# Performance work log

Measured on AMD Instinct MI355X. Metric: run time of the kernel, lower is better.

Reference implementation:

```python
import jax, jax.numpy as jnp
import numpy as np

# Detect.__init__ defaults from the source
TOP_K = 5000
CONF_THRESH = 0.01
NMS_THRESH = 0.3
VAR0, VAR1 = 0.1, 0.2   # variance = [0.1, 0.2]
NUM_CLASSES = 2

B = 16
IMAGE = 1280
FMAPS = [320, 160, 80, 40, 20, 10]          # image / steps [4,8,16,32,64,128]
MIN_SIZES = [16, 32, 64, 128, 256, 512]
AR = 1.5                                     # aspect_ratios = [[1.5]] * 6


def make_priors():
    """Vectorized PriorBox.forward: 1 prior per location (max_sizes=[], single AR)."""
    chunks = []
    for f, ms in zip(FMAPS, MIN_SIZES):
        c = (np.arange(f, dtype=np.float32) + 0.5) / f
        cy, cx = np.meshgrid(c, c, indexing='ij')
        s = ms / float(IMAGE)
        w = np.full_like(cx, s / np.sqrt(AR))   # s_k / sqrt(ar)
        h = np.full_like(cx, s * np.sqrt(AR))   # s_k * sqrt(ar)
        chunks.append(np.stack([cx, cy, w, h], -1).reshape(-1, 4))
    pr = np.concatenate(chunks, 0).clip(0.0, 1.0)   # clip=True
    return jnp.asarray(pr, jnp.float32)             # [136500, 4]


def setup_inputs() -> dict:
    key = jax.random.key(0)
    k1, k2 = jax.random.split(key)
    P = sum(f * f for f in FMAPS)   # 136500
    loc_data = 0.5 * jax.random.normal(k1, (B, P, 4), jnp.float32)
    conf_data = jax.random.uniform(k2, (B * P, NUM_CLASSES), jnp.float32)  # post-softmax probs
    prior_data = make_priors()
    return {"loc_data": loc_data, "conf_data": conf_data, "prior_data": prior_data}


def _decode(loc, priors):
    # SSD box decode with variances [0.1, 0.2]; loc, priors: [P,4]
    cxcy = priors[:, :2] + loc[:, :2] * VAR0 * priors[:, 2:]
    wh = priors[:, 2:] * jnp.exp(loc[:, 2:] * VAR1)
    xy1 = cxcy - wh * 0.5
    xy2 = xy1 + wh
    return jnp.concatenate([xy1, xy2], axis=-1)   # [P,4] x1y1x2y2


def _greedy_keep(boxes, valid):
    # Greedy NMS over score-sorted candidates. boxes [K,4], valid [K] bool.
    # Indices/keep decisions are discrete -> computed on stop_gradient'd boxes.
    b = jax.lax.stop_gradient(boxes)
    x1, y1, x2, y2 = b[:, 0], b[:, 1], b[:, 2], b[:, 3]
    area = (x2 - x1) * (y2 - y1)
    idxs = jnp.arange(b.shape[0])

    def body(keep, i):
        iw = jnp.maximum(jnp.minimum(x2, x2[i]) - jnp.maximum(x1, x1[i]), 0.0)
        ih = jnp.maximum(jnp.minimum(y2, y2[i]) - jnp.maximum(y1, y1[i]), 0.0)
        inter = iw * ih
        iou = inter / (area + area[i] - inter)
        suppress = keep[i] & (iou > NMS_THRESH) & (idxs > i)
        return keep & ~suppress, None

    keep, _ = jax.lax.scan(body, valid, idxs)
    return keep


def _detect_one(loc_i, conf_cl, priors):
    # loc_i [P,4]; conf_cl [P] = class-1 scores; returns [TOP_K, 5] (score, x1,y1,x2,y2)
    boxes = _decode(loc_i, priors)
    masked = jnp.where(conf_cl > CONF_THRESH, conf_cl, -1.0)   # c_mask gating
    order = jnp.argsort(-jax.lax.stop_gradient(masked))[:TOP_K]  # scores.sort, top_k cap
    s = masked[order]
    b = boxes[order]
    valid = s > CONF_THRESH
    keep = _greedy_keep(b, valid)
    # scatter kept (score, box) rows, in descending-score order, into dense output
    rank = jnp.cumsum(keep) - 1
    row = jnp.where(keep, rank, TOP_K)            # dropped rows -> scratch slot
    vals = jnp.concatenate([s[:, None], b], axis=1)
    vals = jnp.where(keep[:, None], vals, 0.0)
    out = jnp.zeros((TOP_K + 1, 5), jnp.float32).at[row].set(vals)
    return out[:TOP_K]


def reference(loc_data, conf_data, prior_data):
    num = loc_data.shape[0]
    P = prior_data.shape[0]
    conf_preds = conf_data.reshape(num, P, NUM_CLASSES).transpose(0, 2, 1)  # [B,2,P]
    cls1 = jax.vmap(_detect_one, in_axes=(0, 0, None))(loc_data, conf_preds[:, 1, :], prior_data)
    bg = jnp.zeros_like(cls1)                     # background class row stays zero
    output = jnp.stack([bg, cls1], axis=1)        # [B, 2, TOP_K, 5]
    # NOTE: the original's final `flt[(rank < top_k)...].fill_(0)` fills a boolean-indexed
    # COPY in torch, so it is a no-op on `output`; we faithfully return output unchanged.
    return output
```

## Files before the change

kernel.cpp:

```cpp
#include <hip/hip_runtime.h>
#include <math.h>

#pragma clang fp contract(off)

#define PNUM 136500
#define HPNUM 68250
#define BNUM 16
#define TOPK 5000
#define CAP 8192
#define NB2 1024
#define B2BASE 0xBC00u
#define NWORDS 79
#define NW32 158
#define GSTRIDE 32
#define CAPE 65536
#define ELDS 10240
#define NXB 128
#define BSTRIDE 5120
#define EBUF 3072

#define OFF_SC    ((size_t)0)
#define OFF_X1    (OFF_SC + 320000)
#define OFF_Y1    (OFF_X1 + 320000)
#define OFF_X2    (OFF_Y1 + 320000)
#define OFF_Y2    (OFF_X2 + 320000)
#define OFF_AREA  (OFF_Y2 + 320000)
#define OFF_HIST  ((size_t)1920000)
#define OFF_CUT   (OFF_HIST + 65536)
#define OFF_SBASE (OFF_CUT + 64)
#define OFF_GBCUR (OFF_SBASE + 65536)
#define OFF_KEYS  (OFF_GBCUR + 1048576)
#define OFF_ECNT  (OFF_KEYS + 1048576)
#define OFF_EDGE  (OFF_ECNT + 2048)
#define OFF_GRP   (OFF_EDGE + 4194304)
#define OFF_BOFS  (OFF_GRP)
#define OFF_SIDX  (OFF_GRP + 16384)
#define OFF_SBOX  (OFF_SIDX + 327680)

__device__ __forceinline__ unsigned f2ord(float f) {
    unsigned u = __float_as_uint(f);
    return (u & 0x80000000u) ? ~u : (u | 0x80000000u);
}
__device__ __forceinline__ float ord2f(unsigned o) {
    unsigned u = (o & 0x80000000u) ? (o ^ 0x80000000u) : ~o;
    return __uint_as_float(u);
}
__device__ __forceinline__ int bucketOf(float x) {
    int b = (int)((x + 0.6f) * 71.111115f);
    return (b < 0) ? 0 : ((b > 127) ? 127 : b);
}

__global__ void __launch_bounds__(256) k_hist(const float* __restrict__ conf,
                                              unsigned* __restrict__ hist) {
    __shared__ unsigned lh[NB2];
    int img = blockIdx.y;
    for (int i = threadIdx.x; i < NB2; i += 256) lh[i] = 0;
    __syncthreads();
    const float4* src = (const float4*)(conf + (size_t)img * PNUM * 2);
    int stride = gridDim.x * 256;
    for (int q = blockIdx.x * 256 + threadIdx.x; q < HPNUM; q += stride) {
        float4 v = src[q];
        if (v.y > 0.01f) atomicAdd(&lh[(f2ord(v.y) >> 16) - B2BASE], 1u);
        if (v.w > 0.01f) atomicAdd(&lh[(f2ord(v.w) >> 16) - B2BASE], 1u);
    }
    __syncthreads();
    unsigned* h = hist + (size_t)img * NB2;
    for (int i = threadIdx.x; i < NB2; i += 256) {
        unsigned c = lh[i];
        if (c) atomicAdd(&h[i], c);
    }
}

__global__ void __launch_bounds__(256) k_cutoff2(const unsigned* __restrict__ hist,
                                                 unsigned* __restrict__ cut,
                                                 unsigned* __restrict__ sbase) {
    __shared__ unsigned csum[256], suf[256];
    int img = blockIdx.x;
    int t = threadIdx.x;
    const unsigned* h = hist + (size_t)img * NB2;
    unsigned h0 = h[t * 4], h1 = h[t * 4 + 1], h2 = h[t * 4 + 2], h3 = h[t * 4 + 3];
    csum[t] = h0 + h1 + h2 + h3;
    __syncthreads();
    if (t == 0) {
        unsigned a = 0;
        for (int g = 255; g >= 0; --g) { unsigned c = csum[g]; suf[g] = a; a += c; }
        unsigned acc = 0, before = 0;
        int c = -1;
        for (int cc = 255; cc >= 0; --cc) {
            if (acc + csum[cc] >= (unsigned)TOPK) { c = cc; before = acc; break; }
            acc += csum[cc];
        }
        unsigned cutb = B2BASE;
        if (c >= 0) {
            unsigned s2 = before;
            cutb = B2BASE + (unsigned)c * 4u;
            for (int b = c * 4 + 3; b >= c * 4; --b) {
                s2 += h[b];
                if (s2 >= (unsigned)TOPK) { cutb = B2BASE + (unsigned)b; break; }
            }
        }
        cut[img] = cutb;
    }
    __syncthreads();
    unsigned a = suf[t];
    unsigned* sb = sbase + (size_t)img * NB2 + t * 4;
    sb[3] = a;
    sb[2] = a + h3;
    sb[1] = a + h3 + h2;
    sb[0] = a + h3 + h2 + h1;
}

__global__ void __launch_bounds__(256) k_gather2(
        const float* __restrict__ conf, const unsigned* __restrict__ cut,
        const unsigned* __restrict__ sbase, unsigned* __restrict__ gbcur,
        unsigned long long* __restrict__ keys) {
    int q = blockIdx.x * 256 + threadIdx.x;
    int img = blockIdx.y;
    if (q >= HPNUM) return;
    unsigned cutb = cut[img];
    float4 v = ((const float4*)(conf + (size_t)img * PNUM * 2))[q];
    const unsigned* sb = sbase + (size_t)img * NB2;
    unsigned* gc = gbcur + (size_t)img * NB2 * 16;
    unsigned long long* kp = keys + (size_t)img * CAP;
    #pragma unroll
    for (int e = 0; e < 2; ++e) {
        float s = e ? v.w : v.y;
        if (s > 0.01f) {
            unsigned o = f2ord(s);
            if ((o >> 16) >= cutb) {
                unsigned wb = (o >> 16) - B2BASE;
                unsigned pos = sb[wb] + atomicAdd(&gc[wb * 16], 1u);
                if (pos < (unsigned)CAP)
                    kp[pos] = ((unsigned long long)o << 32)
                              | (unsigned)(~(unsigned)(2 * q + e));
            }
        }
    }
}

__global__ void __launch_bounds__(256) k_ssort(
        unsigned long long* __restrict__ keys, const unsigned* __restrict__ hist,
        const unsigned* __restrict__ cut, const unsigned* __restrict__ sbase) {
    int img = blockIdx.y;
    int b = blockIdx.x;
    if (B2BASE + (unsigned)b < cut[img]) return;
    unsigned cnt = hist[(size_t)img * NB2 + b];
    if (cnt <= 1) return;
    if (cnt > 1024) cnt = 1024;
    unsigned base = sbase[(size_t)img * NB2 + b];
    __shared__ unsigned long long sk[1024];
    unsigned long long* kp = keys + (size_t)img * CAP + base;
    int tid = threadIdx.x;
    for (int i = tid; i < 1024; i += 256) sk[i] = (i < (int)cnt) ? kp[i] : 0ull;
    __syncthreads();
    for (int k = 2; k <= 1024; k <<= 1) {
        for (int j = k >> 1; j > 0; j >>= 1) {
            for (int t = tid; t < 512; t += 256) {
                int i = ((t & ~(j - 1)) << 1) | (t & (j - 1));
                int p = i | j;
                bool desc = ((i & k) == 0);
                unsigned long long a = sk[i], bb = sk[p];
                bool sw = desc ? (a < bb) : (a > bb);
                if (sw) { sk[i] = bb; sk[p] = a; }
            }
            __syncthreads();
        }
    }
    for (int i = tid; i < (int)cnt; i += 256) kp[i] = sk[i];
}

__global__ void __launch_bounds__(256) k_decode(
        const unsigned long long* __restrict__ keys,
        const float* __restrict__ loc, const float* __restrict__ pri,
        float* __restrict__ SC, float* __restrict__ X1, float* __restrict__ Y1,
        float* __restrict__ X2, float* __restrict__ Y2) {
    int gidx = blockIdx.x * 256 + threadIdx.x;
    if (gidx >= BNUM * TOPK) return;
    int img = gidx / TOPK;
    int r = gidx - img * TOPK;
    unsigned long long key = keys[(size_t)img * CAP + r];
    size_t o = (size_t)img * TOPK + r;
    if (key != 0ull) {
        unsigned ordv = (unsigned)(key >> 32);
        float s = ord2f(ordv);
        unsigned p = ~(unsigned)(key & 0xFFFFFFFFull);
        const float* lp = loc + ((size_t)img * PNUM + p) * 4;
        const float* pp = pri + (size_t)p * 4;
        float lx = lp[0], ly = lp[1], lw = lp[2], lh = lp[3];
        float px = pp[0], py = pp[1], pw = pp[2], ph = pp[3];
        float cx = px + (lx * 0.1f) * pw;
        float cy = py + (ly * 0.1f) * ph;
        float w = pw * expf(lw * 0.2f);
        float h = ph * expf(lh * 0.2f);
        float x1 = cx - w * 0.5f;
        float y1 = cy - h * 0.5f;
        float x2 = x1 + w;
        float y2 = y1 + h;
        SC[o] = s; X1[o] = x1; Y1[o] = y1; X2[o] = x2; Y2[o] = y2;
    } else {
        SC[o] = -1.0f; X1[o] = 0.f; Y1[o] = 0.f; X2[o] = 0.f; Y2[o] = 0.f;
    }
}

__global__ void __launch_bounds__(256) k_bucket(
        const float* __restrict__ X1, const float* __restrict__ X2,
        const float* __restrict__ Y1, const float* __restrict__ Y2,
        unsigned* __restrict__ bofs, unsigned* __restrict__ sidx,
        float4* __restrict__ sbox) {
    __shared__ unsigned bcnt[NXB], bpre[NXB + 1], bcur[NXB];
    int img = blockIdx.x;
    int tid = threadIdx.x;
    if (tid < NXB) bcnt[tid] = 0;
    __syncthreads();
    size_t ib = (size_t)img * TOPK;
    for (int r = tid; r < TOPK; r += 256)
        atomicAdd(&bcnt[bucketOf(X1[ib + r])], 1u);
    __syncthreads();
    if (tid == 0) {
        unsigned a = 0;
        for (int b = 0; b < NXB; ++b) { bpre[b] = a; a += bcnt[b]; }
        bpre[NXB] = a;
    }
    __syncthreads();
    if (tid < NXB) bcur[tid] = bpre[tid];
    if (tid <= NXB) bofs[img * 130 + tid] = bpre[tid];
    __syncthreads();
    int base = img * BSTRIDE;
    for (int r = tid; r < TOPK; r += 256) {
        float x = X1[ib + r];
        unsigned s = atomicAdd(&bcur[bucketOf(x)], 1u);
        sidx[base + s] = (unsigned)r;
        sbox[base + s] = make_float4(x, Y1[ib + r], X2[ib + r], Y2[ib + r]);
    }
}

__global__ void __launch_bounds__(256) k_pair4(
        const unsigned* __restrict__ bofs, const unsigned* __restrict__ sidx,
        const float4* __restrict__ sbox,
        unsigned* __restrict__ ecnt, unsigned* __restrict__ edges) {
    __shared__ unsigned ebuf[EBUF];
    __shared__ unsigned ecl, ebase;
    int img = blockIdx.y;
    int wid = threadIdx.x >> 6;
    int lane = threadIdx.x & 63;
    int sb0 = (blockIdx.x * 4 + wid) * 4;
    if (threadIdx.x == 0) ecl = 0;
    __syncthreads();
    unsigned* ec = ecnt + (size_t)img * GSTRIDE;
    unsigned* eg = edges + (size_t)img * CAPE;
    if (sb0 < TOPK) {
        int base = img * BSTRIDE;
        float x1k[4], x2k[4], y1k[4], y2k[4], ark[4];
        unsigned rk[4];
        bool act[4];
        #pragma unroll
        for (int k = 0; k < 4; ++k) {
            act[k] = (sb0 + k) < TOPK;
            int s = act[k] ? (sb0 + k) : sb0;
            float4 bk = sbox[base + s];
            x1k[k] = bk.x; y1k[k] = bk.y; x2k[k] = bk.z; y2k[k] = bk.w;
            ark[k] = (bk.z - bk.x) * (bk.w - bk.y);
            rk[k] = sidx[base + s];
        }
        int b1 = bucketOf(x1k[0]);
        int b2m = bucketOf(x2k[0]);
        #pragma unroll
        for (int k = 1; k < 4; ++k)
            if (act[k]) { int b = bucketOf(x2k[k]); if (b > b2m) b2m = b; }
        const unsigned* bo = bofs + img * 130;
        unsigned s0 = bo[b1], s1 = bo[b2m + 1];
        if (s0 < s1) {
            unsigned nit = (s1 - s0 + 63) >> 6;
            unsigned c0 = s0 + (unsigned)lane;
            if (c0 > s1 - 1) c0 = s1 - 1;
            float4 cb = sbox[base + c0];
            unsigned cr = sidx[base + c0];
            for (unsigned it = 0; it < nit; ++it) {
                float4 nb = cb; unsigned nr = cr;
                if (it + 1 < nit) {
                    unsigned cn = s0 + (it + 1) * 64 + (unsigned)lane;
                    if (cn > s1 - 1) cn = s1 - 1;
                    nb = sbox[base + cn];
                    nr = sidx[base + cn];
                }
                bool in = (s0 + it * 64 + (unsigned)lane) < s1;
                float bar = (cb.z - cb.x) * (cb.w - cb.y);
                #pragma unroll
                for (int k = 0; k < 4; ++k) {
                    bool hit = false;
                    unsigned edge = 0;
                    if (in && act[k] && cb.x >= x1k[k]
                        && !(cb.x == x1k[k] && cr <= rk[k])) {
                        float dx = fminf(x2k[k], cb.z) - fmaxf(x1k[k], cb.x);
                        if (dx > 0.0f) {
                            float dy = fminf(y2k[k], cb.w) - fmaxf(y1k[k], cb.y);
                            if (dy > 0.0f) {
                                float inter = dx * dy;
                                float iou = inter / (bar + ark[k] - inter);
                                if (iou > 0.3f) {
                                    unsigned su = (rk[k] < cr) ? rk[k] : cr;
                                    unsigned vi = (rk[k] < cr) ? cr : rk[k];
                                    edge = (vi << 13) | su;
                                    hit = true;
                                }
                            }
                        }
                    }
                    unsigned long long bal = __ballot(hit);
                    if (bal) {
                        int n = __popcll(bal);
                        unsigned wb = 0;
                        if (lane == 0) wb = atomicAdd(&ecl, (unsigned)n);
                        wb = __shfl(wb, 0, 64);
                        if (hit) {
                            unsigned long long lt =
                                (lane == 0) ? 0ull : ((1ull << lane) - 1ull);
                            unsigned p = wb + (unsigned)__popcll(bal & lt);
                            if (p < (unsigned)EBUF) ebuf[p] = edge;
                            else {
                                unsigned gp = atomicAdd(ec, 1u);
                                if (gp < (unsigned)CAPE) eg[gp] = edge;
                            }
                        }
                    }
                }
                cb = nb; cr = nr;
            }
        }
    }
    __syncthreads();
    unsigned n = min(ecl, (unsigned)EBUF);
    if (threadIdx.x == 0 && n) ebase = atomicAdd(ec, n);
    __syncthreads();
    for (unsigned i = threadIdx.x; i < n; i += 256) {
        unsigned p = ebase + i;
        if (p < (unsigned)CAPE) eg[p] = ebuf[i];
    }
}

__global__ void __launch_bounds__(256) k_nms3(
        const float* __restrict__ SC, const float* __restrict__ X1,
        const float* __restrict__ Y1, const float* __restrict__ X2,
        const float* __restrict__ Y2,
        const unsigned* __restrict__ ecnt, const unsigned* __restrict__ edges,
        float* __restrict__ out) {
    __shared__ unsigned lgrp[ELDS];
    __shared__ unsigned undL[160], keptL[160], blockL[160];
    __shared__ unsigned pfx[80];
    __shared__ int chg[2];
    int img = blockIdx.x;
    int tid = threadIdx.x;
    int l = tid & 63;
    int wid = tid >> 6;
    size_t ib = (size_t)img * TOPK;
    const float* sc = SC + ib;

    if (tid < 160) { keptL[tid] = 0u; blockL[tid] = 0u; }
    if (tid < 2) chg[tid] = 0;
    for (int w = wid; w < NWORDS; w += 4) {
        int row = w * 64 + l;
        bool valid = (row < TOPK) && (sc[row] > 0.01f);
        unsigned long long b = __ballot(valid);
        if (l == 0) {
            undL[2 * w]     = (unsigned)b;
            undL[2 * w + 1] = (unsigned)(b >> 32);
        }
    }
    unsigned E = min(ecnt[(size_t)img * GSTRIDE], (unsigned)CAPE);
    const unsigned* eimg = edges + (size_t)img * CAPE;
    bool inl = (E <= (unsigned)ELDS);
    if (inl) for (unsigned e = tid; e < E; e += 256) lgrp[e] = eimg[e];
    __syncthreads();

    for (int round = 0; round < 256; ++round) {
        int par = round & 1;
        for (unsigned e = tid; e < E; e += 256) {
            unsigned ed = inl ? lgrp[e] : eimg[e];
            unsigned s = ed & 8191u;
            unsigned v = ed >> 13;
            unsigned sw = s >> 5, sb = s & 31u;
            unsigned vw = v >> 5, vb = 1u << (v & 31u);
            if ((keptL[sw] >> sb) & 1u) {
                if (undL[vw] & vb) {
                    unsigned old = atomicAnd(&undL[vw], ~vb);
                    if (old & vb) chg[par] = 1;
                }
            } else if ((undL[sw] >> sb) & 1u) {
                if (!(blockL[vw] & vb)) atomicOr(&blockL[vw], vb);
            }
        }
        __syncthreads();
        if (tid < NW32) {
            unsigned nk = undL[tid] & ~blockL[tid];
            if (nk) {
                keptL[tid] |= nk;
                undL[tid] &= ~nk;
                chg[par] = 1;
            }
            blockL[tid] = 0u;
        }
        if (tid == 0) chg[par ^ 1] = 0;
        __syncthreads();
        if (!chg[par]) break;
    }

    if (tid == 0) {
        unsigned acc = 0;
        for (int w = 0; w < NWORDS; ++w) {
            pfx[w] = acc;
            acc += (unsigned)(__popc(keptL[2 * w]) + __popc(keptL[2 * w + 1]));
        }
    }
    __syncthreads();
    const float* x1 = X1 + ib; const float* y1 = Y1 + ib;
    const float* x2 = X2 + ib; const float* y2 = Y2 + ib;
    float* op = out + (((size_t)img * 2) + 1) * TOPK * 5;
    for (int w = wid; w < NWORDS; w += 4) {
        unsigned long long kw =
            ((unsigned long long)keptL[2 * w + 1] << 32) | keptL[2 * w];
        if (!kw) continue;
        int row = w * 64 + l;
        if ((kw >> l) & 1ull) {
            int rank = (int)pfx[w] + (int)__popcll(kw & ((1ull << l) - 1ull));
            float* r = op + (size_t)rank * 5;
            r[0] = sc[row]; r[1] = x1[row]; r[2] = y1[row];
            r[3] = x2[row]; r[4] = y2[row];
        }
    }
}

extern "C" void kernel_launch(void* const* d_in, const int* in_sizes, int n_in,
                              void* d_out, int out_size, void* d_ws, size_t ws_size,
                              hipStream_t stream) {
    (void)in_sizes; (void)n_in; (void)ws_size;
    const float* loc  = (const float*)d_in[0];
    const float* conf = (const float*)d_in[1];
    const float* pri  = (const float*)d_in[2];
    float* out = (float*)d_out;
    char* ws = (char*)d_ws;

    float* SC   = (float*)(ws + OFF_SC);
    float* X1   = (float*)(ws + OFF_X1);
    float* Y1   = (float*)(ws + OFF_Y1);
    float* X2   = (float*)(ws + OFF_X2);
    float* Y2   = (float*)(ws + OFF_Y2);
    unsigned* hist = (unsigned*)(ws + OFF_HIST);
    unsigned* cut  = (unsigned*)(ws + OFF_CUT);
    unsigned* sbase = (unsigned*)(ws + OFF_SBASE);
    unsigned* gbcur = (unsigned*)(ws + OFF_GBCUR);
    unsigned long long* keys = (unsigned long long*)(ws + OFF_KEYS);
    unsigned* ecnt = (unsigned*)(ws + OFF_ECNT);
    unsigned* edges = (unsigned*)(ws + OFF_EDGE);
    unsigned* bofs = (unsigned*)(ws + OFF_BOFS);
    unsigned* sidx = (unsigned*)(ws + OFF_SIDX);
    float4* sbox = (float4*)(ws + OFF_SBOX);

    hipMemsetAsync(d_out, 0, (size_t)out_size * sizeof(float), stream);
    hipMemsetAsync(ws + OFF_HIST, 0, (OFF_ECNT + 2048) - OFF_HIST, stream);

    dim3 gh1(16, BNUM);
    k_hist<<<gh1, 256, 0, stream>>>(conf, hist);
    k_cutoff2<<<BNUM, 256, 0, stream>>>(hist, cut, sbase);
    dim3 gh2((HPNUM + 255) / 256, BNUM);
    k_gather2<<<gh2, 256, 0, stream>>>(conf, cut, sbase, gbcur, keys);
    dim3 gs(NB2, BNUM);
    k_ssort<<<gs, 256, 0, stream>>>(keys, hist, cut, sbase);
    k_decode<<<(BNUM * TOPK + 255) / 256, 256, 0, stream>>>(
        keys, loc, pri, SC, X1, Y1, X2, Y2);

    k_bucket<<<BNUM, 256, 0, stream>>>(X1, X2, Y1, Y2, bofs, sidx, sbox);
    dim3 pg((TOPK + 15) / 16, BNUM);
    k_pair4<<<pg, 256, 0, stream>>>(bofs, sidx, sbox, ecnt, edges);
    k_nms3<<<BNUM, 256, 0, stream>>>(SC, X1, Y1, X2, Y2, ecnt, edges, out);
}
```

Measured before the change: 243.9 us.

## Drop workspace memset, use per-block histograms, fuse bucket counting into decode

The histogram kernel now writes per-block partial histograms that the cutoff kernel sums, replacing global atomics. The cutoff kernel also zeroes the gbcur region (reused for the partials), ecnt and the new bucket counters, which removes the large workspace memset. Box coordinates are stored as one float4 array instead of four SoA arrays, and decode counts the x-buckets with global atomics. The single-block-per-image bucket kernel becomes a multi-block scatter, which makes the order of boxes within each bucket nondeterministic.

```diff
diff --git a/kernel.cpp b/kernel.cpp
--- a/kernel.cpp
+++ b/kernel.cpp
@@ -18,20 +18,19 @@
 #define NXB 128
 #define BSTRIDE 5120
 #define EBUF 3072
+#define NHB 16
 
 #define OFF_SC    ((size_t)0)
-#define OFF_X1    (OFF_SC + 320000)
-#define OFF_Y1    (OFF_X1 + 320000)
-#define OFF_X2    (OFF_Y1 + 320000)
-#define OFF_Y2    (OFF_X2 + 320000)
-#define OFF_AREA  (OFF_Y2 + 320000)
+#define OFF_BOX4  (OFF_SC + 320000)
 #define OFF_HIST  ((size_t)1920000)
 #define OFF_CUT   (OFF_HIST + 65536)
 #define OFF_SBASE (OFF_CUT + 64)
 #define OFF_GBCUR (OFF_SBASE + 65536)
 #define OFF_KEYS  (OFF_GBCUR + 1048576)
 #define OFF_ECNT  (OFF_KEYS + 1048576)
-#define OFF_EDGE  (OFF_ECNT + 2048)
+#define OFF_BCNT  (OFF_ECNT + 2048)
+#define OFF_BCUR  (OFF_BCNT + 8192)
+#define OFF_EDGE  (OFF_BCUR + 8192)
 #define OFF_GRP   (OFF_EDGE + 4194304)
 #define OFF_BOFS  (OFF_GRP)
 #define OFF_SIDX  (OFF_GRP + 16384)
@@ -51,7 +50,7 @@
 }
 
 __global__ void __launch_bounds__(256) k_hist(const float* __restrict__ conf,
-                                              unsigned* __restrict__ hist) {
+                                              unsigned* __restrict__ parts) {
     __shared__ unsigned lh[NB2];
     int img = blockIdx.y;
     for (int i = threadIdx.x; i < NB2; i += 256) lh[i] = 0;
@@ -64,23 +63,33 @@
         if (v.w > 0.01f) atomicAdd(&lh[(f2ord(v.w) >> 16) - B2BASE], 1u);
     }
     __syncthreads();
-    unsigned* h = hist + (size_t)img * NB2;
-    for (int i = threadIdx.x; i < NB2; i += 256) {
-        unsigned c = lh[i];
-        if (c) atomicAdd(&h[i], c);
-    }
-}
-
-__global__ void __launch_bounds__(256) k_cutoff2(const unsigned* __restrict__ hist,
-                                                 unsigned* __restrict__ cut,
-                                                 unsigned* __restrict__ sbase) {
+    unsigned* p = parts + ((size_t)img * NHB + blockIdx.x) * NB2;
+    for (int i = threadIdx.x; i < NB2; i += 256) p[i] = lh[i];
+}
+
+__global__ void __launch_bounds__(256) k_cutoff2(
+        unsigned* __restrict__ parts,
+        unsigned* __restrict__ shist, unsigned* __restrict__ cut,
+        unsigned* __restrict__ sbase, unsigned* __restrict__ ecnt,
+        unsigned* __restrict__ bcnt, unsigned* __restrict__ bcur) {
     __shared__ unsigned csum[256], suf[256];
     int img = blockIdx.x;
     int t = threadIdx.x;
-    const unsigned* h = hist + (size_t)img * NB2;
-    unsigned h0 = h[t * 4], h1 = h[t * 4 + 1], h2 = h[t * 4 + 2], h3 = h[t * 4 + 3];
+    const unsigned* pp = parts + (size_t)img * NHB * NB2;
+    unsigned h0 = 0, h1 = 0, h2 = 0, h3 = 0;
+    #pragma unroll
+    for (int blk = 0; blk < NHB; ++blk) {
+        const unsigned* q = pp + blk * NB2 + t * 4;
+        h0 += q[0]; h1 += q[1]; h2 += q[2]; h3 += q[3];
+    }
     csum[t] = h0 + h1 + h2 + h3;
-    __syncthreads();
+    unsigned* sh = shist + (size_t)img * NB2;
+    sh[t * 4] = h0; sh[t * 4 + 1] = h1; sh[t * 4 + 2] = h2; sh[t * 4 + 3] = h3;
+    __syncthreads();
+    unsigned* gc = parts + (size_t)img * NB2 * 16;
+    for (int i = t; i < NB2 * 16; i += 256) gc[i] = 0;
+    if (t < GSTRIDE) ecnt[img * GSTRIDE + t] = 0;
+    if (t < NXB) { bcnt[img * NXB + t] = 0; bcur[img * NXB + t] = 0; }
     if (t == 0) {
         unsigned a = 0;
         for (int g = 255; g >= 0; --g) { unsigned c = csum[g]; suf[g] = a; a += c; }
@@ -95,7 +104,7 @@
             unsigned s2 = before;
             cutb = B2BASE + (unsigned)c * 4u;
             for (int b = c * 4 + 3; b >= c * 4; --b) {
-                s2 += h[b];
+                s2 += sh[b];
                 if (s2 >= (unsigned)TOPK) { cutb = B2BASE + (unsigned)b; break; }
             }
         }
@@ -172,17 +181,18 @@
 __global__ void __launch_bounds__(256) k_decode(
         const unsigned long long* __restrict__ keys,
         const float* __restrict__ loc, const float* __restrict__ pri,
-        float* __restrict__ SC, float* __restrict__ X1, float* __restrict__ Y1,
-        float* __restrict__ X2, float* __restrict__ Y2) {
+        float* __restrict__ SC, float4* __restrict__ BOX4,
+        unsigned* __restrict__ bcnt) {
     int gidx = blockIdx.x * 256 + threadIdx.x;
     if (gidx >= BNUM * TOPK) return;
     int img = gidx / TOPK;
     int r = gidx - img * TOPK;
     unsigned long long key = keys[(size_t)img * CAP + r];
     size_t o = (size_t)img * TOPK + r;
+    float s, x1, y1, x2, y2;
     if (key != 0ull) {
         unsigned ordv = (unsigned)(key >> 32);
-        float s = ord2f(ordv);
+        s = ord2f(ordv);
         unsigned p = ~(unsigned)(key & 0xFFFFFFFFull);
         const float* lp = loc + ((size_t)img * PNUM + p) * 4;
         const float* pp = pri + (size_t)p * 4;
@@ -192,45 +202,43 @@
         float cy = py + (ly * 0.1f) * ph;
         float w = pw * expf(lw * 0.2f);
         float h = ph * expf(lh * 0.2f);
-        float x1 = cx - w * 0.5f;
-        float y1 = cy - h * 0.5f;
-        float x2 = x1 + w;
-        float y2 = y1 + h;
-        SC[o] = s; X1[o] = x1; Y1[o] = y1; X2[o] = x2; Y2[o] = y2;
+        x1 = cx - w * 0.5f;
+        y1 = cy - h * 0.5f;
+        x2 = x1 + w;
+        y2 = y1 + h;
     } else {
-        SC[o] = -1.0f; X1[o] = 0.f; Y1[o] = 0.f; X2[o] = 0.f; Y2[o] = 0.f;
-    }
-}
-
-__global__ void __launch_bounds__(256) k_bucket(
-        const float* __restrict__ X1, const float* __restrict__ X2,
-        const float* __restrict__ Y1, const float* __restrict__ Y2,
+        s = -1.0f; x1 = 0.f; y1 = 0.f; x2 = 0.f; y2 = 0.f;
+    }
+    SC[o] = s;
+    BOX4[o] = make_float4(x1, y1, x2, y2);
+    atomicAdd(&bcnt[img * NXB + bucketOf(x1)], 1u);
+}
+
+__global__ void __launch_bounds__(256) k_bscat(
+        const unsigned* __restrict__ bcnt, unsigned* __restrict__ bcur,
+        const float4* __restrict__ BOX4,
         unsigned* __restrict__ bofs, unsigned* __restrict__ sidx,
         float4* __restrict__ sbox) {
-    __shared__ unsigned bcnt[NXB], bpre[NXB + 1], bcur[NXB];
-    int img = blockIdx.x;
+    __shared__ unsigned lc[NXB], bpre[NXB + 1];
+    int img = blockIdx.y;
     int tid = threadIdx.x;
-    if (tid < NXB) bcnt[tid] = 0;
-    __syncthreads();
-    size_t ib = (size_t)img * TOPK;
-    for (int r = tid; r < TOPK; r += 256)
-        atomicAdd(&bcnt[bucketOf(X1[ib + r])], 1u);
+    if (tid < NXB) lc[tid] = bcnt[img * NXB + tid];
     __syncthreads();
     if (tid == 0) {
         unsigned a = 0;
-        for (int b = 0; b < NXB; ++b) { bpre[b] = a; a += bcnt[b]; }
+        for (int b = 0; b < NXB; ++b) { bpre[b] = a; a += lc[b]; }
         bpre[NXB] = a;
     }
     __syncthreads();
-    if (tid < NXB) bcur[tid] = bpre[tid];
-    if (tid <= NXB) bofs[img * 130 + tid] = bpre[tid];
-    __syncthreads();
-    int base = img * BSTRIDE;
-    for (int r = tid; r < TOPK; r += 256) {
-        float x = X1[ib + r];
-        unsigned s = atomicAdd(&bcur[bucketOf(x)], 1u);
+    if (blockIdx.x == 0 && tid <= NXB) bofs[img * 130 + tid] = bpre[tid];
+    int r = blockIdx.x * 256 + tid;
+    if (r < TOPK) {
+        float4 b = BOX4[(size_t)img * TOPK + r];
+        int bk = bucketOf(b.x);
+        unsigned s = bpre[bk] + atomicAdd(&bcur[img * NXB + bk], 1u);
+        int base = img * BSTRIDE;
         sidx[base + s] = (unsigned)r;
-        sbox[base + s] = make_float4(x, Y1[ib + r], X2[ib + r], Y2[ib + r]);
+        sbox[base + s] = b;
     }
 }
 
@@ -339,9 +347,7 @@
 }
 
 __global__ void __launch_bounds__(256) k_nms3(
-        const float* __restrict__ SC, const float* __restrict__ X1,
-        const float* __restrict__ Y1, const float* __restrict__ X2,
-        const float* __restrict__ Y2,
+        const float* __restrict__ SC, const float4* __restrict__ BOX4,
         const unsigned* __restrict__ ecnt, const unsigned* __restrict__ edges,
         float* __restrict__ out) {
     __shared__ unsigned lgrp[ELDS];
@@ -412,8 +418,7 @@
         }
     }
     __syncthreads();
-    const float* x1 = X1 + ib; const float* y1 = Y1 + ib;
-    const float* x2 = X2 + ib; const float* y2 = Y2 + ib;
+    const float4* bx = BOX4 + ib;
     float* op = out + (((size_t)img * 2) + 1) * TOPK * 5;
     for (int w = wid; w < NWORDS; w += 4) {
         unsigned long long kw =
@@ -422,9 +427,9 @@
         int row = w * 64 + l;
         if ((kw >> l) & 1ull) {
             int rank = (int)pfx[w] + (int)__popcll(kw & ((1ull << l) - 1ull));
+            float4 b = bx[row];
             float* r = op + (size_t)rank * 5;
-            r[0] = sc[row]; r[1] = x1[row]; r[2] = y1[row];
-            r[3] = x2[row]; r[4] = y2[row];
+            r[0] = sc[row]; r[1] = b.x; r[2] = b.y; r[3] = b.z; r[4] = b.w;
         }
     }
 }
@@ -440,36 +445,35 @@
     char* ws = (char*)d_ws;
 
     float* SC   = (float*)(ws + OFF_SC);
-    float* X1   = (float*)(ws + OFF_X1);
-    float* Y1   = (float*)(ws + OFF_Y1);
-    float* X2   = (float*)(ws + OFF_X2);
-    float* Y2   = (float*)(ws + OFF_Y2);
-    unsigned* hist = (unsigned*)(ws + OFF_HIST);
+    float4* BOX4 = (float4*)(ws + OFF_BOX4);
+    unsigned* shist = (unsigned*)(ws + OFF_HIST);
     unsigned* cut  = (unsigned*)(ws + OFF_CUT);
     unsigned* sbase = (unsigned*)(ws + OFF_SBASE);
     unsigned* gbcur = (unsigned*)(ws + OFF_GBCUR);
     unsigned long long* keys = (unsigned long long*)(ws + OFF_KEYS);
     unsigned* ecnt = (unsigned*)(ws + OFF_ECNT);
+    unsigned* bcnt = (unsigned*)(ws + OFF_BCNT);
+    unsigned* bcur = (unsigned*)(ws + OFF_BCUR);
     unsigned* edges = (unsigned*)(ws + OFF_EDGE);
     unsigned* bofs = (unsigned*)(ws + OFF_BOFS);
     unsigned* sidx = (unsigned*)(ws + OFF_SIDX);
     float4* sbox = (float4*)(ws + OFF_SBOX);
 
     hipMemsetAsync(d_out, 0, (size_t)out_size * sizeof(float), stream);
-    hipMemsetAsync(ws + OFF_HIST, 0, (OFF_ECNT + 2048) - OFF_HIST, stream);
-
-    dim3 gh1(16, BNUM);
-    k_hist<<<gh1, 256, 0, stream>>>(conf, hist);
-    k_cutoff2<<<BNUM, 256, 0, stream>>>(hist, cut, sbase);
+
+    dim3 gh1(NHB, BNUM);
+    k_hist<<<gh1, 256, 0, stream>>>(conf, gbcur);
+    k_cutoff2<<<BNUM, 256, 0, stream>>>(gbcur, shist, cut, sbase,
+                                        ecnt, bcnt, bcur);
     dim3 gh2((HPNUM + 255) / 256, BNUM);
     k_gather2<<<gh2, 256, 0, stream>>>(conf, cut, sbase, gbcur, keys);
     dim3 gs(NB2, BNUM);
-    k_ssort<<<gs, 256, 0, stream>>>(keys, hist, cut, sbase);
+    k_ssort<<<gs, 256, 0, stream>>>(keys, shist, cut, sbase);
     k_decode<<<(BNUM * TOPK + 255) / 256, 256, 0, stream>>>(
-        keys, loc, pri, SC, X1, Y1, X2, Y2);
-
-    k_bucket<<<BNUM, 256, 0, stream>>>(X1, X2, Y1, Y2, bofs, sidx, sbox);
+        keys, loc, pri, SC, BOX4, bcnt);
+    dim3 gb((TOPK + 255) / 256, BNUM);
+    k_bscat<<<gb, 256, 0, stream>>>(bcnt, bcur, BOX4, bofs, sidx, sbox);
     dim3 pg((TOPK + 15) / 16, BNUM);
     k_pair4<<<pg, 256, 0, stream>>>(bofs, sidx, sbox, ecnt, edges);
-    k_nms3<<<BNUM, 256, 0, stream>>>(SC, X1, Y1, X2, Y2, ecnt, edges, out);
-}
+    k_nms3<<<BNUM, 256, 0, stream>>>(SC, BOX4, ecnt, edges, out);
+}
```

After: 251.8 us. +3.2%, slower.
